# Kernel tuning notes

Hardware: AMD Instinct MI355X
Metric: run time of the kernel (lower is better)

Reference implementation:

```python
import jax, jax.numpy as jnp
import numpy as np

B, N = 2048, 8192
K = 64          # subset size / number of relaxation steps
TAU = 1.0
EPS = 1e-10


def setup_inputs() -> dict:
    key = jax.random.key(0)
    k1, k2 = jax.random.split(key)
    scores = jax.random.normal(k1, (B, N), dtype=jnp.float32)
    # Gumbel(0,1) noise, same as torch.distributions.Gumbel(zeros, ones).sample()
    u = jax.random.uniform(k2, (B, N), dtype=jnp.float32, minval=1e-20, maxval=1.0)
    g = -jnp.log(-jnp.log(u))
    return {"scores": scores, "g": g}


def reference(scores, g):
    # Perturb scores with Gumbel noise
    s0 = scores + g  # [B, N]
    khot0 = jnp.zeros_like(s0)
    onehot0 = jnp.zeros_like(s0)

    def step(carry, _):
        s, khot, onehot_approx = carry
        khot_mask = jnp.maximum(1.0 - onehot_approx, EPS)   # suppress picked items
        s = s + jnp.log(khot_mask)
        onehot_approx = jax.nn.softmax(s / TAU, axis=1)
        return (s, khot + onehot_approx, onehot_approx), None

    (_, khot, _), _ = jax.lax.scan(step, (s0, khot0, onehot0), None, length=K)
    # hard=False -> return relaxed k-hot vector
    return khot
```

## Files before the change

kernel.cpp:

```cpp
#include <hip/hip_runtime.h>
#include <math.h>


#define BROWS 2048
#define NCOLS 8192
#define KSTEPS 64

#define THREADS 256
#define EPT (NCOLS / THREADS)

__global__ __launch_bounds__(THREADS, 4) void gumbel_subset_kernel(
    const float* __restrict__ scores,
    const float* __restrict__ g,
    float* __restrict__ out)
{
    const int row = blockIdx.x;
    const int t = threadIdx.x;
    const float* __restrict__ srow = scores + (size_t)row * NCOLS;
    const float* __restrict__ grow = g + (size_t)row * NCOLS;
    float* __restrict__ orow = out + (size_t)row * NCOLS;

    float v[EPT];
    float kh[EPT];

    float m = -INFINITY;
#pragma unroll
    for (int c = 0; c < EPT / 4; ++c) {
        const int idx = c * (THREADS * 4) + t * 4;
        const float4 a = *reinterpret_cast<const float4*>(srow + idx);
        const float4 b = *reinterpret_cast<const float4*>(grow + idx);
        const float s0 = a.x + b.x;
        const float s1 = a.y + b.y;
        const float s2 = a.z + b.z;
        const float s3 = a.w + b.w;
        v[c * 4 + 0] = s0;
        v[c * 4 + 1] = s1;
        v[c * 4 + 2] = s2;
        v[c * 4 + 3] = s3;
        m = fmaxf(m, fmaxf(fmaxf(s0, s1), fmaxf(s2, s3)));
    }

    __shared__ float red[2][8];
    const int wave = t >> 6;
    const int lane = t & 63;

#pragma unroll
    for (int off = 32; off > 0; off >>= 1)
        m = fmaxf(m, __shfl_xor(m, off, 64));
    if (lane == 0) red[0][wave] = m;
    __syncthreads();
    m = fmaxf(fmaxf(red[0][0], red[0][1]), fmaxf(red[0][2], red[0][3]));
    __syncthreads();

#pragma unroll
    for (int e = 0; e < EPT; ++e) {
        v[e] = __expf(v[e] - m);
        kh[e] = 0.0f;
    }

#pragma unroll 2
    for (int it = 0; it < KSTEPS; ++it) {
        float s = 0.0f;
#pragma unroll
        for (int e = 0; e < EPT; ++e) s += v[e];
#pragma unroll
        for (int off = 32; off > 0; off >>= 1)
            s += __shfl_xor(s, off, 64);

        const int buf = it & 1;
        if (lane == 0) red[buf][wave] = s;
        __syncthreads();
        const float S = (red[buf][0] + red[buf][1]) + (red[buf][2] + red[buf][3]);
        const float rinv = __builtin_amdgcn_rcpf(S);

#pragma unroll
        for (int e = 0; e < EPT; ++e) {
            const float w = v[e] * rinv;
            kh[e] += w;
            v[e] = __builtin_fmaf(-w, v[e], v[e]);
        }
    }

#pragma unroll
    for (int c = 0; c < EPT / 4; ++c) {
        const int idx = c * (THREADS * 4) + t * 4;
        float4 o;
        o.x = kh[c * 4 + 0];
        o.y = kh[c * 4 + 1];
        o.z = kh[c * 4 + 2];
        o.w = kh[c * 4 + 3];
        *reinterpret_cast<float4*>(orow + idx) = o;
    }
}

extern "C" void kernel_launch(void* const* d_in, const int* in_sizes, int n_in,
                              void* d_out, int out_size, void* d_ws, size_t ws_size,
                              hipStream_t stream) {
    const float* scores = (const float*)d_in[0];
    const float* g = (const float*)d_in[1];
    float* out = (float*)d_out;
    (void)in_sizes; (void)n_in; (void)out_size; (void)d_ws; (void)ws_size;

    gumbel_subset_kernel<<<BROWS, THREADS, 0, stream>>>(scores, g, out);
}
```

Before: 110.6 us.

## Process one row per wave with packed fp16 state and fused sum

Each wavefront now owns a whole row, so the per-step block reduction and __syncthreads go away and only a wave shuffle remains. Per-element state (v and the k-hot accumulator) is held as packed half2 and updated with v_pk_mul/v_pk_fma inline asm, which halves register use and doubles ALU throughput. The sum for the next step is computed inside the update loop, so no separate pass over v is needed. Inputs are read twice (once for the max, once for the exp) so that fp32 values need not be kept, and fp16 state adds rounding error in both the weights and the accumulated k-hot values.

```diff
diff --git a/kernel.cpp b/kernel.cpp
--- a/kernel.cpp
+++ b/kernel.cpp
@@ -1,94 +1,102 @@
 #include <hip/hip_runtime.h>
 #include <math.h>
 
+
+typedef _Float16 h2 __attribute__((ext_vector_type(2)));
 
 #define BROWS 2048
 #define NCOLS 8192
 #define KSTEPS 64
 
 #define THREADS 256
-#define EPT (NCOLS / THREADS)
+#define WPB 4
+#define EPL (NCOLS / 64)
+#define NPK (EPL / 2)
+#define NACC 16
 
-__global__ __launch_bounds__(THREADS, 4) void gumbel_subset_kernel(
+__global__ __launch_bounds__(THREADS, 2) void gumbel_subset_kernel(
     const float* __restrict__ scores,
     const float* __restrict__ g,
     float* __restrict__ out)
 {
-    const int row = blockIdx.x;
-    const int t = threadIdx.x;
+    const int wave = threadIdx.x >> 6;
+    const int lane = threadIdx.x & 63;
+    const int row = blockIdx.x * WPB + wave;
     const float* __restrict__ srow = scores + (size_t)row * NCOLS;
     const float* __restrict__ grow = g + (size_t)row * NCOLS;
     float* __restrict__ orow = out + (size_t)row * NCOLS;
 
-    float v[EPT];
-    float kh[EPT];
-
     float m = -INFINITY;
 #pragma unroll
-    for (int c = 0; c < EPT / 4; ++c) {
-        const int idx = c * (THREADS * 4) + t * 4;
+    for (int c = 0; c < EPL / 4; ++c) {
+        const int idx = c * 256 + lane * 4;
         const float4 a = *reinterpret_cast<const float4*>(srow + idx);
         const float4 b = *reinterpret_cast<const float4*>(grow + idx);
-        const float s0 = a.x + b.x;
-        const float s1 = a.y + b.y;
-        const float s2 = a.z + b.z;
-        const float s3 = a.w + b.w;
-        v[c * 4 + 0] = s0;
-        v[c * 4 + 1] = s1;
-        v[c * 4 + 2] = s2;
-        v[c * 4 + 3] = s3;
-        m = fmaxf(m, fmaxf(fmaxf(s0, s1), fmaxf(s2, s3)));
+        m = fmaxf(m, fmaxf(fmaxf(a.x + b.x, a.y + b.y),
+                           fmaxf(a.z + b.z, a.w + b.w)));
     }
-
-    __shared__ float red[2][8];
-    const int wave = t >> 6;
-    const int lane = t & 63;
-
 #pragma unroll
     for (int off = 32; off > 0; off >>= 1)
         m = fmaxf(m, __shfl_xor(m, off, 64));
-    if (lane == 0) red[0][wave] = m;
-    __syncthreads();
-    m = fmaxf(fmaxf(red[0][0], red[0][1]), fmaxf(red[0][2], red[0][3]));
-    __syncthreads();
 
+    h2 v[NPK];
+    h2 kh[NPK];
+    float part = 0.0f;
 #pragma unroll
-    for (int e = 0; e < EPT; ++e) {
-        v[e] = __expf(v[e] - m);
-        kh[e] = 0.0f;
+    for (int c = 0; c < EPL / 4; ++c) {
+        const int idx = c * 256 + lane * 4;
+        const float4 a = *reinterpret_cast<const float4*>(srow + idx);
+        const float4 b = *reinterpret_cast<const float4*>(grow + idx);
+        const float e0 = __expf(a.x + b.x - m);
+        const float e1 = __expf(a.y + b.y - m);
+        const float e2 = __expf(a.z + b.z - m);
+        const float e3 = __expf(a.w + b.w - m);
+        v[2 * c + 0] = (h2){(_Float16)e0, (_Float16)e1};
+        v[2 * c + 1] = (h2){(_Float16)e2, (_Float16)e3};
+        kh[2 * c + 0] = (h2){(_Float16)0.0f, (_Float16)0.0f};
+        kh[2 * c + 1] = (h2){(_Float16)0.0f, (_Float16)0.0f};
+        part += (e0 + e1) + (e2 + e3);
     }
 
-#pragma unroll 2
     for (int it = 0; it < KSTEPS; ++it) {
-        float s = 0.0f;
-#pragma unroll
-        for (int e = 0; e < EPT; ++e) s += v[e];
+        float s = part;
 #pragma unroll
         for (int off = 32; off > 0; off >>= 1)
             s += __shfl_xor(s, off, 64);
 
-        const int buf = it & 1;
-        if (lane == 0) red[buf][wave] = s;
-        __syncthreads();
-        const float S = (red[buf][0] + red[buf][1]) + (red[buf][2] + red[buf][3]);
-        const float rinv = __builtin_amdgcn_rcpf(S);
+        const float rinv = __builtin_amdgcn_rcpf(s);
+        const h2 rn2 = (h2){(_Float16)(-rinv), (_Float16)(-rinv)};
+        const h2 n1 = (h2){(_Float16)(-1.0f), (_Float16)(-1.0f)};
 
+        float partf = 0.0f;
 #pragma unroll
-        for (int e = 0; e < EPT; ++e) {
-            const float w = v[e] * rinv;
-            kh[e] += w;
-            v[e] = __builtin_fmaf(-w, v[e], v[e]);
+        for (int grp = 0; grp < NACC; ++grp) {
+            h2 acc = (h2){(_Float16)0.0f, (_Float16)0.0f};
+#pragma unroll
+            for (int j = 0; j < 4; ++j) {
+                const int p = grp * 4 + j;
+                h2 nw, kn, vn, an;
+                asm("v_pk_mul_f16 %0, %1, %2" : "=&v"(nw) : "v"(v[p]), "v"(rn2));
+                asm("v_pk_fma_f16 %0, %1, %2, %3" : "=&v"(kn) : "v"(nw), "v"(n1), "v"(kh[p]));
+                kh[p] = kn;
+                asm("v_pk_fma_f16 %0, %1, %2, %3" : "=&v"(vn) : "v"(nw), "v"(v[p]), "v"(v[p]));
+                v[p] = vn;
+                asm("v_pk_add_f16 %0, %1, %2" : "=&v"(an) : "v"(acc), "v"(v[p]));
+                acc = an;
+            }
+            partf += (float)acc.x + (float)acc.y;
         }
+        part = partf;
     }
 
 #pragma unroll
-    for (int c = 0; c < EPT / 4; ++c) {
-        const int idx = c * (THREADS * 4) + t * 4;
+    for (int c = 0; c < EPL / 4; ++c) {
+        const int idx = c * 256 + lane * 4;
         float4 o;
-        o.x = kh[c * 4 + 0];
-        o.y = kh[c * 4 + 1];
-        o.z = kh[c * 4 + 2];
-        o.w = kh[c * 4 + 3];
+        o.x = (float)kh[2 * c + 0].x;
+        o.y = (float)kh[2 * c + 0].y;
+        o.z = (float)kh[2 * c + 1].x;
+        o.w = (float)kh[2 * c + 1].y;
         *reinterpret_cast<float4*>(orow + idx) = o;
     }
 }
@@ -101,5 +109,5 @@
     float* out = (float*)d_out;
     (void)in_sizes; (void)n_in; (void)out_size; (void)d_ws; (void)ws_size;
 
-    gumbel_subset_kernel<<<BROWS, THREADS, 0, stream>>>(scores, g, out);
+    gumbel_subset_kernel<<<BROWS / WPB, THREADS, 0, stream>>>(scores, g, out);
 }
```

Result: slower. 139.4 us (+26.0%).
